# Kernel tuning notes

Hardware: AMD Instinct MI355X
Metric: run time of the kernel (lower is better)

## Reference

```python
import jax, jax.numpy as jnp
import numpy as np
import math

B, T, C, H = 2, 2048, 1024, 16
HD = C // H  # head dim = 64

def setup_inputs() -> dict:
    key = jax.random.key(0)
    ks = jax.random.split(key, 12)
    s = 0.02
    return {
        "x": jax.random.normal(ks[0], (B, T, C), dtype=jnp.float32),
        "ln1_g": jnp.ones((C,), jnp.float32),
        "ln1_b": jnp.zeros((C,), jnp.float32),
        "W_attn": jax.random.normal(ks[1], (C, 3 * C), jnp.float32) * s,
        "b_attn": jnp.zeros((3 * C,), jnp.float32),
        "W_ap": jax.random.normal(ks[2], (C, C), jnp.float32) * s,
        "b_ap": jnp.zeros((C,), jnp.float32),
        "ln2_g": jnp.ones((C,), jnp.float32),
        "ln2_b": jnp.zeros((C,), jnp.float32),
        "W_fc": jax.random.normal(ks[3], (C, 4 * C), jnp.float32) * s,
        "b_fc": jnp.zeros((4 * C,), jnp.float32),
        "W_mp": jax.random.normal(ks[4], (4 * C, C), jnp.float32) * s,
        "b_mp": jnp.zeros((C,), jnp.float32),
    }

def layernorm(x, g, b, eps=1e-5):
    mu = jnp.mean(x, axis=-1, keepdims=True)
    var = jnp.mean(jnp.square(x - mu), axis=-1, keepdims=True)
    return (x - mu) * jax.lax.rsqrt(var + eps) * g + b

def gelu_tanh(x):
    # GELU(approximate='tanh')
    c = math.sqrt(2.0 / math.pi)
    return 0.5 * x * (1.0 + jnp.tanh(c * (x + 0.044715 * x * x * x)))

def attention(x, W_attn, b_attn, W_ap, b_ap):
    b, t, c = x.shape
    qkv = x @ W_attn + b_attn                      # [B,T,3C]
    q, k, v = jnp.split(qkv, 3, axis=-1)
    q = q.reshape(b, t, H, HD).transpose(0, 2, 1, 3)  # [B,H,T,hd]
    k = k.reshape(b, t, H, HD).transpose(0, 2, 1, 3)
    v = v.reshape(b, t, H, HD).transpose(0, 2, 1, 3)
    attn = jnp.einsum('bhqd,bhkd->bhqk', q, k) * (1.0 / math.sqrt(HD))
    mask = jnp.tril(jnp.ones((t, t), dtype=bool))
    attn = jnp.where(mask, attn, jnp.float32(-jnp.inf))
    attn = jax.nn.softmax(attn, axis=-1)
    y = jnp.einsum('bhqk,bhkd->bhqd', attn, v)
    y = y.transpose(0, 2, 1, 3).reshape(b, t, c)
    return y @ W_ap + b_ap

def reference(x, ln1_g, ln1_b, W_attn, b_attn, W_ap, b_ap,
              ln2_g, ln2_b, W_fc, b_fc, W_mp, b_mp):
    x = x + attention(layernorm(x, ln1_g, ln1_b), W_attn, b_attn, W_ap, b_ap)
    h = layernorm(x, ln2_g, ln2_b)
    h = gelu_tanh(h @ W_fc + b_fc) @ W_mp + b_mp
    return x + h
```

## Files before the change

kernel.cpp:

```cpp
#include <hip/hip_runtime.h>
#include <stdint.h>

#define TT_ 2048
#define CC_ 1024

typedef unsigned short u16;
typedef __bf16 bf16x8 __attribute__((ext_vector_type(8)));
typedef float f32x4 __attribute__((ext_vector_type(4)));
typedef unsigned short u16x8 __attribute__((ext_vector_type(8)));

__device__ __forceinline__ u16 f2bf(float f) {
  unsigned u = __float_as_uint(f);
  u += 0x7fff + ((u >> 16) & 1);
  return (u16)(u >> 16);
}

__device__ __forceinline__ float gelu_f(float t) {
  float u = 1.5957691216057308f * (t + 0.044715f * t * t * t);
  return t / (1.f + __expf(-u));
}

__device__ __forceinline__ void async_cp16(const u16* g, u16* l) {
  __builtin_amdgcn_global_load_lds(
      (const __attribute__((address_space(1))) void*)(uintptr_t)g,
      (__attribute__((address_space(3))) void*)(uint32_t)(uintptr_t)l,
      16, 0, 0);
}

__device__ __forceinline__ void blockbar() {
  asm volatile("" ::: "memory");
  __builtin_amdgcn_s_barrier();
  asm volatile("" ::: "memory");
}

__global__ __launch_bounds__(256) void kconv_t(const float* __restrict__ W,
                                               u16* __restrict__ WT, int K, int N) {
  __shared__ float t[32][33];
  int n0 = blockIdx.x * 32, k0 = blockIdx.y * 32;
  int tx = threadIdx.x & 31, ty = threadIdx.x >> 5;
#pragma unroll
  for (int r = 0; r < 4; ++r)
    t[ty + 8 * r][tx] = W[(size_t)(k0 + ty + 8 * r) * N + n0 + tx];
  __syncthreads();
#pragma unroll
  for (int r = 0; r < 4; ++r)
    WT[(size_t)(n0 + ty + 8 * r) * K + k0 + tx] = f2bf(t[tx][ty + 8 * r]);
}

__global__ __launch_bounds__(256) void kln(const float* __restrict__ x,
                                           const float* __restrict__ g,
                                           const float* __restrict__ b,
                                           u16* __restrict__ out) {
  int row = blockIdx.x, tid = threadIdx.x;
  const float4* xr = (const float4*)(x + (size_t)row * CC_);
  float4 v = xr[tid];
  float s = v.x + v.y + v.z + v.w;
  float s2 = v.x * v.x + v.y * v.y + v.z * v.z + v.w * v.w;
#pragma unroll
  for (int off = 32; off; off >>= 1) { s += __shfl_down(s, off); s2 += __shfl_down(s2, off); }
  __shared__ float rs[4], rq[4];
  int w = tid >> 6;
  if ((tid & 63) == 0) { rs[w] = s; rq[w] = s2; }
  __syncthreads();
  s = rs[0] + rs[1] + rs[2] + rs[3];
  s2 = rq[0] + rq[1] + rq[2] + rq[3];
  float mean = s * (1.f / CC_);
  float var = s2 * (1.f / CC_) - mean * mean;
  float rstd = rsqrtf(var + 1e-5f);
  float4 gv = ((const float4*)g)[tid];
  float4 bv = ((const float4*)b)[tid];
  u16* orow = out + (size_t)row * CC_ + tid * 4;
  orow[0] = f2bf((v.x - mean) * rstd * gv.x + bv.x);
  orow[1] = f2bf((v.y - mean) * rstd * gv.y + bv.y);
  orow[2] = f2bf((v.z - mean) * rstd * gv.z + bv.z);
  orow[3] = f2bf((v.w - mean) * rstd * gv.w + bv.w);
}

template <int EPI, int NSPLIT>
__global__ __launch_bounds__(256) void kgemm(const u16* __restrict__ A,
                                             const u16* __restrict__ BTm,
                                             const float* __restrict__ bias,
                                             const float* __restrict__ resid,
                                             void* __restrict__ out,
                                             float* __restrict__ part,
                                             int M, int N, int Ktot) {
  __shared__ __align__(16) u16 As[2][128 * 32];
  __shared__ __align__(16) u16 Bs[2][128 * 32];
  const int tid = threadIdx.x, lane = tid & 63, w = tid >> 6;
  const int llo = lane & 15, lhi = lane >> 4;
  const int row0 = blockIdx.y * 128, col0 = blockIdx.x * 128;
  const int wr = w >> 1, wc = w & 1;
  const int crow = lane >> 2;
  const int ck = (lane & 3) * 8;
  const int Kc = Ktot / NSPLIT;
  const int klo = (NSPLIT > 1) ? blockIdx.z * Kc : 0;

  f32x4 acc[4][4] = {};

  auto stage = [&](int bufi, int kof) {
#pragma unroll
    for (int c = w; c < 8; c += 4) {
      int r = c * 16 + crow;
      async_cp16(A + (size_t)(row0 + r) * Ktot + klo + kof + ck, &As[bufi][c * 512]);
      async_cp16(BTm + (size_t)(col0 + r) * Ktot + klo + kof + ck, &Bs[bufi][c * 512]);
    }
  };

  const int nt = Kc / 32;
  stage(0, 0);
  asm volatile("s_waitcnt vmcnt(0)" ::: "memory");
  blockbar();
  int cur = 0;

  for (int t = 0; t < nt; ++t) {
    if (t + 1 < nt) stage(cur ^ 1, (t + 1) * 32);
    bf16x8 af[4], bfr[4];
#pragma unroll
    for (int m = 0; m < 4; ++m)
      af[m] = *(const bf16x8*)&As[cur][(wr * 64 + m * 16 + llo) * 32 + lhi * 8];
#pragma unroll
    for (int n = 0; n < 4; ++n)
      bfr[n] = *(const bf16x8*)&Bs[cur][(wc * 64 + n * 16 + llo) * 32 + lhi * 8];
#pragma unroll
    for (int m = 0; m < 4; ++m)
#pragma unroll
      for (int n = 0; n < 4; ++n)
        acc[m][n] = __builtin_amdgcn_mfma_f32_16x16x32_bf16(af[m], bfr[n], acc[m][n], 0, 0, 0);
    if (t + 1 < nt) {
      asm volatile("s_waitcnt vmcnt(0)" ::: "memory");
      blockbar();
    }
    cur ^= 1;
  }

  const int c_row = row0 + wr * 64 + lhi * 4;
  const int c_col = col0 + wc * 64 + llo;
  const bool fin = (NSPLIT == 1) || (blockIdx.z == 0);
#pragma unroll
  for (int n = 0; n < 4; ++n) {
    int col = c_col + n * 16;
    float bb = bias[col];
#pragma unroll
    for (int m = 0; m < 4; ++m) {
      f32x4 a = acc[m][n];
#pragma unroll
      for (int i = 0; i < 4; ++i) {
        size_t idx = (size_t)(c_row + m * 16 + i) * N + col;
        if (!fin) {
          part[idx] = a[i];
        } else {
          float val = a[i] + bb;
          if constexpr (EPI == 1) {
            ((float*)out)[idx] = val + resid[idx];
          } else if constexpr (EPI == 2) {
            ((u16*)out)[idx] = f2bf(gelu_f(val));
          } else {
            ((u16*)out)[idx] = f2bf(val);
          }
        }
      }
    }
  }
}

__global__ __launch_bounds__(256) void kadd(float* __restrict__ out,
                                            const float* __restrict__ part) {
  size_t i = ((size_t)blockIdx.x * 256 + threadIdx.x) * 4;
  float4 o = *(float4*)(out + i);
  float4 p = *(const float4*)(part + i);
  o.x += p.x; o.y += p.y; o.z += p.z; o.w += p.w;
  *(float4*)(out + i) = o;
}

__global__ __launch_bounds__(256) void kvtrans(const u16* __restrict__ qkv,
                                               u16* __restrict__ VT) {
  int tt = blockIdx.x;
  int bh = blockIdx.y;
  int b = bh >> 4, h = bh & 15;
  __shared__ u16 t[64][72];
  int r = threadIdx.x >> 3, c0 = (threadIdx.x & 7) * 8;
  const u16* src = qkv + (size_t)(b * TT_ + tt * 64) * 3072 + 2048 + h * 64;
#pragma unroll
  for (int it = 0; it < 2; ++it) {
    int rr = r + it * 32;
    *(u16x8*)&t[rr][c0] = *(const u16x8*)(src + (size_t)rr * 3072 + c0);
  }
  __syncthreads();
  u16* dst = VT + ((size_t)bh * 64) * TT_ + tt * 64;
#pragma unroll
  for (int it = 0; it < 2; ++it) {
    int d = r + it * 32;
    u16x8 v;
#pragma unroll
    for (int e = 0; e < 8; ++e) v[e] = t[c0 + e][d];
    *(u16x8*)(dst + (size_t)d * TT_ + c0) = v;
  }
}

__global__ __launch_bounds__(512, 4) void kattn(const u16* __restrict__ qkv,
                                                const u16* __restrict__ VT,
                                                u16* __restrict__ y) {
  const int h = blockIdx.x, b = blockIdx.y;
  const int qt = 15 - blockIdx.z;
  const int tid = threadIdx.x, lane = tid & 63, w = tid >> 6;
  const int llo = lane & 15, lhi = lane >> 4;

  __shared__ __align__(16) u16 Qs[128 * 64];
  __shared__ __align__(16) u16 Ks[2][64 * 64];
  __shared__ __align__(16) u16 Vs[2][64 * 64];
  __shared__ __align__(16) u16 Ps[128 * 72];

  const size_t tok0 = (size_t)b * TT_;
  const int q0 = qt * 128;
  const u16* qb = qkv + tok0 * 3072 + h * 64;
  const u16* kb = qb + 1024;

  {
    int r8 = tid >> 3, ce = (tid & 7) * 8;
#pragma unroll
    for (int it = 0; it < 2; ++it) {
      int tk = it * 64 + r8;
      u16x8 v = *(const u16x8*)(qb + (size_t)(q0 + tk) * 3072 + ce);
      *(u16x8*)&Qs[tk * 64 + (ce ^ ((tk & 7) << 3))] = v;
    }
  }
  asm volatile("s_waitcnt lgkmcnt(0)" ::: "memory");

  const int srow = lane >> 3;
  const int scol = ((lane & 7) * 8) ^ ((srow & 7) << 3);
  const u16* kg = kb + (size_t)(w * 8 + srow) * 3072 + scol;
  const u16* vg = VT + ((size_t)(b * 16 + h) * 64 + w * 8 + srow) * TT_ + scol;

  const int ntiles = 2 * qt + 2;
  async_cp16(kg, &Ks[0][w * 512]);
  async_cp16(vg, &Vs[0][w * 512]);

  blockbar();

  bf16x8 aq[2];
#pragma unroll
  for (int kk = 0; kk < 2; ++kk)
    aq[kk] = *(const bf16x8*)&Qs[(w * 16 + llo) * 64 + ((kk * 32 + lhi * 8) ^ ((llo & 7) << 3))];

  float m_i[4], l_i[4];
  f32x4 o[4] = {};
#pragma unroll
  for (int i = 0; i < 4; ++i) { m_i[i] = -1e30f; l_i[i] = 0.f; }

  const int row_min = q0 + w * 16, row_max = row_min + 15;
  int buf = 0;

  for (int j = 0; j < ntiles; ++j) {
    if (j + 1 < ntiles) {
      async_cp16(kg + (size_t)(j + 1) * (64 * 3072), &Ks[buf ^ 1][w * 512]);
      async_cp16(vg + (size_t)(j + 1) * 64, &Vs[buf ^ 1][w * 512]);
      asm volatile("s_waitcnt vmcnt(2)" ::: "memory");
    } else {
      asm volatile("s_waitcnt vmcnt(0)" ::: "memory");
    }
    blockbar();

    const int kmin = j * 64;
    if (kmin <= row_max) {
      f32x4 s[4] = {};
#pragma unroll
      for (int nb = 0; nb < 4; ++nb)
#pragma unroll
        for (int kk = 0; kk < 2; ++kk) {
          bf16x8 bk = *(const bf16x8*)&Ks[buf][(nb * 16 + llo) * 64 +
                                              ((kk * 32 + lhi * 8) ^ ((llo & 7) << 3))];
          s[nb] = __builtin_amdgcn_mfma_f32_16x16x32_bf16(aq[kk], bk, s[nb], 0, 0, 0);
        }

      const bool part = (kmin + 63 > row_min);
      float sc[4][4];
#pragma unroll
      for (int nb = 0; nb < 4; ++nb)
#pragma unroll
        for (int i = 0; i < 4; ++i) {
          float v = s[nb][i] * 0.125f;
          if (part && (kmin + nb * 16 + llo > row_min + lhi * 4 + i)) v = -1e30f;
          sc[nb][i] = v;
        }

#pragma unroll
      for (int i = 0; i < 4; ++i) {
        float rm = fmaxf(fmaxf(sc[0][i], sc[1][i]), fmaxf(sc[2][i], sc[3][i]));
#pragma unroll
        for (int off = 1; off < 16; off <<= 1) rm = fmaxf(rm, __shfl_xor(rm, off));
        float mnew = fmaxf(m_i[i], rm);
        float corr = __expf(m_i[i] - mnew);
        float p0 = __expf(sc[0][i] - mnew);
        float p1 = __expf(sc[1][i] - mnew);
        float p2 = __expf(sc[2][i] - mnew);
        float p3 = __expf(sc[3][i] - mnew);
        float rsum = p0 + p1 + p2 + p3;
#pragma unroll
        for (int off = 1; off < 16; off <<= 1) rsum += __shfl_xor(rsum, off);
        l_i[i] = l_i[i] * corr + rsum;
        m_i[i] = mnew;
#pragma unroll
        for (int db = 0; db < 4; ++db) o[db][i] *= corr;
        u16* pr = &Ps[(w * 16 + lhi * 4 + i) * 72 + llo];
        pr[0] = f2bf(p0); pr[16] = f2bf(p1); pr[32] = f2bf(p2); pr[48] = f2bf(p3);
      }

      bf16x8 pa[2];
#pragma unroll
      for (int kk = 0; kk < 2; ++kk)
        pa[kk] = *(const bf16x8*)&Ps[(w * 16 + llo) * 72 + kk * 32 + lhi * 8];
#pragma unroll
      for (int db = 0; db < 4; ++db)
#pragma unroll
        for (int kk = 0; kk < 2; ++kk) {
          bf16x8 bv = *(const bf16x8*)&Vs[buf][(db * 16 + llo) * 64 +
                                              ((kk * 32 + lhi * 8) ^ ((llo & 7) << 3))];
          o[db] = __builtin_amdgcn_mfma_f32_16x16x32_bf16(pa[kk], bv, o[db], 0, 0, 0);
        }
    }
    blockbar();
    buf ^= 1;
  }

#pragma unroll
  for (int i = 0; i < 4; ++i) {
    float inv = 1.f / l_i[i];
    size_t row = tok0 + q0 + w * 16 + lhi * 4 + i;
#pragma unroll
    for (int db = 0; db < 4; ++db)
      y[row * CC_ + h * 64 + db * 16 + llo] = f2bf(o[db][i] * inv);
  }
}

extern "C" void kernel_launch(void* const* d_in, const int* in_sizes, int n_in,
                              void* d_out, int out_size, void* d_ws, size_t ws_size,
                              hipStream_t stream) {
  (void)in_sizes; (void)n_in; (void)out_size; (void)ws_size;
  const float* x      = (const float*)d_in[0];
  const float* ln1g   = (const float*)d_in[1];
  const float* ln1b   = (const float*)d_in[2];
  const float* W_attn = (const float*)d_in[3];
  const float* b_attn = (const float*)d_in[4];
  const float* W_ap   = (const float*)d_in[5];
  const float* b_ap   = (const float*)d_in[6];
  const float* ln2g   = (const float*)d_in[7];
  const float* ln2b   = (const float*)d_in[8];
  const float* W_fc   = (const float*)d_in[9];
  const float* b_fc   = (const float*)d_in[10];
  const float* W_mp   = (const float*)d_in[11];
  const float* b_mp   = (const float*)d_in[12];

  char* p = (char*)d_ws;
  u16* WTattn = (u16*)p; p += (size_t)3072 * 1024 * 2;
  u16* WTap   = (u16*)p; p += (size_t)1024 * 1024 * 2;
  u16* WTfc   = (u16*)p; p += (size_t)4096 * 1024 * 2;
  u16* WTmp   = (u16*)p; p += (size_t)4096 * 1024 * 2;
  u16* xn     = (u16*)p; p += (size_t)4096 * 1024 * 2;
  u16* qkvb   = (u16*)p; p += (size_t)4096 * 3072 * 2;
  u16* yb     = (u16*)p; p += (size_t)4096 * 1024 * 2;
  float* x1   = (float*)p; p += (size_t)4096 * 1024 * 4;
  u16* h2     = (u16*)p; p += (size_t)4096 * 1024 * 2;
  u16* fcb    = qkvb;
  u16* VT     = (u16*)x1;
  float* mppart = (float*)d_ws;

  kconv_t<<<dim3(96, 32), 256, 0, stream>>>(W_attn, WTattn, 1024, 3072);
  kconv_t<<<dim3(32, 32), 256, 0, stream>>>(W_ap, WTap, 1024, 1024);
  kconv_t<<<dim3(128, 32), 256, 0, stream>>>(W_fc, WTfc, 1024, 4096);
  kconv_t<<<dim3(32, 128), 256, 0, stream>>>(W_mp, WTmp, 4096, 1024);

  kln<<<4096, 256, 0, stream>>>(x, ln1g, ln1b, xn);
  kgemm<0, 1><<<dim3(24, 32), 256, 0, stream>>>(xn, WTattn, b_attn, nullptr, qkvb, nullptr, 4096, 3072, 1024);
  kvtrans<<<dim3(32, 32), 256, 0, stream>>>(qkvb, VT);
  kattn<<<dim3(16, 2, 16), 512, 0, stream>>>(qkvb, VT, yb);
  kgemm<1, 1><<<dim3(8, 32), 256, 0, stream>>>(yb, WTap, b_ap, x, x1, nullptr, 4096, 1024, 1024);
  kln<<<4096, 256, 0, stream>>>(x1, ln2g, ln2b, h2);
  kgemm<2, 1><<<dim3(32, 32), 256, 0, stream>>>(h2, WTfc, b_fc, nullptr, fcb, nullptr, 4096, 4096, 1024);
  kgemm<1, 2><<<dim3(8, 32, 2), 256, 0, stream>>>(fcb, WTmp, b_mp, x1, (float*)d_out, mppart, 4096, 1024, 4096);
  kadd<<<4096, 256, 0, stream>>>((float*)d_out, mppart);
}
```

Baseline: 283.5 us.

## Rework attention softmax: prescaled exp2, lazy rescale, permuted K rows, packed P stores

Folds the 1/sqrt(d)·log2(e) factor into Q at load time so the softmax uses exp2 with no per-score multiply. The running max and output are rescaled only when some row's max grows by more than 8. K rows are loaded in a permuted order so each lane's four score columns are contiguous, which lets P be written to shared memory as packed 64-bit stores instead of scattered 16-bit ones. It also raises wave priority around the MFMA blocks and interleaves the causal q-tile ordering across the grid for load balance. Risks: an extra bf16 rounding of the scaled Q, and bounded growth of unnormalised P values before a rescale.

```diff
diff --git a/kernel.cpp b/kernel.cpp
--- a/kernel.cpp
+++ b/kernel.cpp
@@ -8,11 +8,15 @@
 typedef __bf16 bf16x8 __attribute__((ext_vector_type(8)));
 typedef float f32x4 __attribute__((ext_vector_type(4)));
 typedef unsigned short u16x8 __attribute__((ext_vector_type(8)));
+typedef unsigned int u32x2 __attribute__((ext_vector_type(2)));
 
 __device__ __forceinline__ u16 f2bf(float f) {
   unsigned u = __float_as_uint(f);
   u += 0x7fff + ((u >> 16) & 1);
   return (u16)(u >> 16);
+}
+__device__ __forceinline__ float bf2f(u16 v) {
+  return __uint_as_float(((unsigned)v) << 16);
 }
 
 __device__ __forceinline__ float gelu_f(float t) {
@@ -201,7 +205,8 @@
                                                 const u16* __restrict__ VT,
                                                 u16* __restrict__ y) {
   const int h = blockIdx.x, b = blockIdx.y;
-  const int qt = 15 - blockIdx.z;
+  const int z = blockIdx.z;
+  const int qt = (z < 8) ? (15 - z) : (z - 8);
   const int tid = threadIdx.x, lane = tid & 63, w = tid >> 6;
   const int llo = lane & 15, lhi = lane >> 4;
 
@@ -216,20 +221,24 @@
   const u16* kb = qb + 1024;
 
   {
+    const float alpha = 0.18033688011112042f;
     int r8 = tid >> 3, ce = (tid & 7) * 8;
 #pragma unroll
     for (int it = 0; it < 2; ++it) {
       int tk = it * 64 + r8;
       u16x8 v = *(const u16x8*)(qb + (size_t)(q0 + tk) * 3072 + ce);
+#pragma unroll
+      for (int e = 0; e < 8; ++e) v[e] = f2bf(bf2f(v[e]) * alpha);
       *(u16x8*)&Qs[tk * 64 + (ce ^ ((tk & 7) << 3))] = v;
     }
   }
   asm volatile("s_waitcnt lgkmcnt(0)" ::: "memory");
 
-  const int srow = lane >> 3;
-  const int scol = ((lane & 7) * 8) ^ ((srow & 7) << 3);
-  const u16* kg = kb + (size_t)(w * 8 + srow) * 3072 + scol;
-  const u16* vg = VT + ((size_t)(b * 16 + h) * 64 + w * 8 + srow) * TT_ + scol;
+  const int p_ = w * 8 + (lane >> 3);
+  const int krow = ((p_ & 15) << 2) | (p_ >> 4);
+  const int scol = ((lane & 7) * 8) ^ ((p_ & 7) << 3);
+  const u16* kg = kb + (size_t)krow * 3072 + scol;
+  const u16* vg = VT + ((size_t)(b * 16 + h) * 64 + p_) * TT_ + scol;
 
   const int ntiles = 2 * qt + 2;
   async_cp16(kg, &Ks[0][w * 512]);
@@ -263,6 +272,7 @@
     const int kmin = j * 64;
     if (kmin <= row_max) {
       f32x4 s[4] = {};
+      __builtin_amdgcn_s_setprio(1);
 #pragma unroll
       for (int nb = 0; nb < 4; ++nb)
 #pragma unroll
@@ -271,6 +281,7 @@
                                               ((kk * 32 + lhi * 8) ^ ((llo & 7) << 3))];
           s[nb] = __builtin_amdgcn_mfma_f32_16x16x32_bf16(aq[kk], bk, s[nb], 0, 0, 0);
         }
+      __builtin_amdgcn_s_setprio(0);
 
       const bool part = (kmin + 63 > row_min);
       float sc[4][4];
@@ -278,37 +289,55 @@
       for (int nb = 0; nb < 4; ++nb)
 #pragma unroll
         for (int i = 0; i < 4; ++i) {
-          float v = s[nb][i] * 0.125f;
-          if (part && (kmin + nb * 16 + llo > row_min + lhi * 4 + i)) v = -1e30f;
+          float v = s[nb][i];
+          if (part && (kmin + llo * 4 + nb > row_min + lhi * 4 + i)) v = -1e30f;
           sc[nb][i] = v;
         }
 
+      float rm[4];
 #pragma unroll
       for (int i = 0; i < 4; ++i) {
-        float rm = fmaxf(fmaxf(sc[0][i], sc[1][i]), fmaxf(sc[2][i], sc[3][i]));
-#pragma unroll
-        for (int off = 1; off < 16; off <<= 1) rm = fmaxf(rm, __shfl_xor(rm, off));
-        float mnew = fmaxf(m_i[i], rm);
-        float corr = __expf(m_i[i] - mnew);
-        float p0 = __expf(sc[0][i] - mnew);
-        float p1 = __expf(sc[1][i] - mnew);
-        float p2 = __expf(sc[2][i] - mnew);
-        float p3 = __expf(sc[3][i] - mnew);
-        float rsum = p0 + p1 + p2 + p3;
+        float r = fmaxf(fmaxf(sc[0][i], sc[1][i]), fmaxf(sc[2][i], sc[3][i]));
+#pragma unroll
+        for (int off = 1; off < 16; off <<= 1) r = fmaxf(r, __shfl_xor(r, off));
+        rm[i] = r;
+      }
+
+      bool need = (rm[0] > m_i[0] + 8.f) | (rm[1] > m_i[1] + 8.f) |
+                  (rm[2] > m_i[2] + 8.f) | (rm[3] > m_i[3] + 8.f);
+      if (__any(need)) {
+#pragma unroll
+        for (int i = 0; i < 4; ++i) {
+          float mn = fmaxf(m_i[i], rm[i]);
+          float corr = exp2f(m_i[i] - mn);
+          l_i[i] *= corr;
+#pragma unroll
+          for (int db = 0; db < 4; ++db) o[db][i] *= corr;
+          m_i[i] = mn;
+        }
+      }
+
+#pragma unroll
+      for (int i = 0; i < 4; ++i) {
+        float p0 = exp2f(sc[0][i] - m_i[i]);
+        float p1 = exp2f(sc[1][i] - m_i[i]);
+        float p2 = exp2f(sc[2][i] - m_i[i]);
+        float p3 = exp2f(sc[3][i] - m_i[i]);
+        float rsum = (p0 + p1) + (p2 + p3);
 #pragma unroll
         for (int off = 1; off < 16; off <<= 1) rsum += __shfl_xor(rsum, off);
-        l_i[i] = l_i[i] * corr + rsum;
-        m_i[i] = mnew;
-#pragma unroll
-        for (int db = 0; db < 4; ++db) o[db][i] *= corr;
-        u16* pr = &Ps[(w * 16 + lhi * 4 + i) * 72 + llo];
-        pr[0] = f2bf(p0); pr[16] = f2bf(p1); pr[32] = f2bf(p2); pr[48] = f2bf(p3);
+        l_i[i] += rsum;
+        u32x2 pk;
+        pk[0] = (unsigned)f2bf(p0) | ((unsigned)f2bf(p1) << 16);
+        pk[1] = (unsigned)f2bf(p2) | ((unsigned)f2bf(p3) << 16);
+        *(u32x2*)&Ps[(w * 16 + lhi * 4 + i) * 72 + llo * 4] = pk;
       }
 
       bf16x8 pa[2];
 #pragma unroll
       for (int kk = 0; kk < 2; ++kk)
         pa[kk] = *(const bf16x8*)&Ps[(w * 16 + llo) * 72 + kk * 32 + lhi * 8];
+      __builtin_amdgcn_s_setprio(1);
 #pragma unroll
       for (int db = 0; db < 4; ++db)
 #pragma unroll
@@ -317,6 +346,7 @@
                                               ((kk * 32 + lhi * 8) ^ ((llo & 7) << 3))];
           o[db] = __builtin_amdgcn_mfma_f32_16x16x32_bf16(pa[kk], bv, o[db], 0, 0, 0);
         }
+      __builtin_amdgcn_s_setprio(0);
     }
     blockbar();
     buf ^= 1;
```

Measured after the change: 279.4 us. Within noise of the previous version (-1.4%).
